# Kernel tuning notes

Hardware: AMD Instinct MI355X
Metric: run time of the kernel (lower is better)

Reference implementation:

```python
import jax, jax.numpy as jnp
import numpy as np

H, W = 32, 56
CK, CV = 64, 512
N = 16 * H * W  # long + work memory fully populated: 16 frames of H*W entries
TOP_K = 30


def setup_inputs() -> dict:
    key = jax.random.key(0)
    k1, k2, k3, k4, k5 = jax.random.split(key, 5)
    return {
        "q_key": jax.random.normal(k1, (1, CK, H, W), dtype=jnp.float32),
        "q_selection": jax.random.uniform(k2, (1, CK, H, W), dtype=jnp.float32),
        "mem_key": jax.random.normal(k3, (1, CK, N), dtype=jnp.float32),
        "mem_shrinkage": jax.random.uniform(k4, (1, N, 1), dtype=jnp.float32),
        "mem_value": jax.random.normal(k5, (2, CV, N), dtype=jnp.float32),
    }


def reference(q_key, q_selection, mem_key, mem_shrinkage, mem_value):
    b, ck, h, w = q_key.shape
    hw = h * w
    qk = q_key.reshape(1, ck, hw)          # [1, CK, HW]
    qs = q_selection.reshape(1, ck, hw)    # [1, CK, HW]

    mk = jnp.swapaxes(mem_key, 1, 2)       # [1, N, CK]
    # negative weighted squared L2 distance via matmul algebra
    a_sq = jnp.matmul(mk * mk, qs)                    # [1, N, HW]
    two_ab = 2.0 * jnp.matmul(mk, qk * qs)            # [1, N, HW]
    b_sq = jnp.sum(qs * qk * qk, axis=1, keepdims=True)  # [1, 1, HW]
    sim = (-a_sq + two_ab - b_sq) * mem_shrinkage / jnp.sqrt(jnp.float32(ck))  # [1, N, HW]

    # topk over the memory axis (dim=1), softmax over selected entries, scatter back
    simT = jnp.swapaxes(sim, 1, 2)                    # [1, HW, N]
    vals, idx = jax.lax.top_k(simT, TOP_K)            # [1, HW, K]
    x_exp = jnp.exp(vals)
    x_exp = x_exp / jnp.sum(x_exp, axis=-1, keepdims=True)
    i0 = jnp.arange(1)[:, None, None]
    i1 = jnp.arange(hw)[None, :, None]
    affT = jnp.zeros_like(simT).at[i0, i1, idx].set(x_exp)  # [1, HW, N]
    affinity = jnp.swapaxes(affT, 1, 2)               # [1, N, HW]

    out = jnp.matmul(mem_value, affinity)             # [2, CV, HW] (batch-broadcast)
    return out.reshape(2, CV, h, w)
```

## Files before the change

### kernel.cpp

```cpp
#include <hip/hip_runtime.h>
#include <math.h>

#define HW      1792
#define NMEM    28672
#define NCHUNK  3584
#define TOPK    30
#define KSEL    48
#define SCAP    64
#define SIMB    448
#define WPS     7

typedef __attribute__((ext_vector_type(8))) short bf16x8;
typedef __attribute__((ext_vector_type(8))) unsigned short u16x8;
typedef __attribute__((ext_vector_type(4))) float f32x4;
typedef __attribute__((ext_vector_type(4))) _Float16 h4;
typedef unsigned long long ull;

static __device__ __forceinline__ unsigned short f2bf(float v) {
  unsigned b = __float_as_uint(v);
  return (unsigned short)((b + 0x7FFFu + ((b >> 16) & 1u)) >> 16);
}
static __device__ __forceinline__ float bf2f(unsigned short h) {
  return __uint_as_float(((unsigned)h) << 16);
}
static __device__ __forceinline__ unsigned fkey(float v) {
  return __float_as_uint(-v) & 0x7FFFFFFFu;
}
static __device__ __forceinline__ ull umax64(ull a, ull b) { return a > b ? a : b; }
static __device__ __forceinline__ ull umin64(ull a, ull b) { return a < b ? a : b; }
static __device__ __forceinline__ void gl_lds16(const void* g, void* l) {
  __builtin_amdgcn_global_load_lds(
      (const __attribute__((address_space(1))) unsigned*)g,
      (__attribute__((address_space(3))) unsigned*)l, 16, 0, 0);
}
#define WSYNC() do { asm volatile("s_waitcnt lgkmcnt(0)" ::: "memory"); \
                     __builtin_amdgcn_wave_barrier(); } while (0)

__global__ __launch_bounds__(256)
void k_prep_b(const float* __restrict__ mk, const float* __restrict__ shr_in,
              unsigned short* __restrict__ Bh,
              float* __restrict__ mkT, float* __restrict__ shr_s)
{
  const int n = blockIdx.x * 256 + threadIdx.x;
  shr_s[n] = shr_in[n] * 0.125f;
  for (int cb = 0; cb < 64; cb += 8) {
    u16x8 h1, h2;
    float vv[8];
    #pragma unroll
    for (int j = 0; j < 8; ++j) {
      float v = mk[(size_t)(cb + j) * NMEM + n];
      vv[j] = v;
      h1[j] = f2bf(v);
      h2[j] = f2bf(v * v);
    }
    const int s = cb >> 3;
    *reinterpret_cast<u16x8*>(&Bh[((size_t)s * NMEM + n) * 8])       = h1;
    *reinterpret_cast<u16x8*>(&Bh[((size_t)(s + 8) * NMEM + n) * 8]) = h2;
    *reinterpret_cast<float4*>(&mkT[(size_t)n * 64 + cb])     = make_float4(vv[0], vv[1], vv[2], vv[3]);
    *reinterpret_cast<float4*>(&mkT[(size_t)n * 64 + cb + 4]) = make_float4(vv[4], vv[5], vv[6], vv[7]);
  }
}

__global__ __launch_bounds__(256)
void k_prep_u(const float* __restrict__ q_key, const float* __restrict__ q_sel,
              unsigned short* __restrict__ Uh, unsigned short* __restrict__ Ul,
              float* __restrict__ bsq)
{
  const int p = blockIdx.x * 256 + threadIdx.x;
  float bs = 0.f;
  for (int cb = 0; cb < 64; cb += 8) {
    u16x8 h1, l1, h2, l2;
    #pragma unroll
    for (int j = 0; j < 8; ++j) {
      int c = cb + j;
      float k = q_key[(size_t)c * HW + p];
      float s = q_sel[(size_t)c * HW + p];
      float u = 2.f * k * s;
      float w = -s;
      bs = fmaf(s * k, k, bs);
      unsigned short h = f2bf(u); h1[j] = h; l1[j] = f2bf(u - bf2f(h));
      unsigned short g = f2bf(w); h2[j] = g; l2[j] = f2bf(w - bf2f(g));
    }
    const int s = cb >> 3;
    *reinterpret_cast<u16x8*>(&Uh[((size_t)s * HW + p) * 8])       = h1;
    *reinterpret_cast<u16x8*>(&Ul[((size_t)s * HW + p) * 8])       = l1;
    *reinterpret_cast<u16x8*>(&Uh[((size_t)(s + 8) * HW + p) * 8]) = h2;
    *reinterpret_cast<u16x8*>(&Ul[((size_t)(s + 8) * HW + p) * 8]) = l2;
  }
  bsq[p] = bs;
}

__global__ __launch_bounds__(256, 2)
void k_sim(const unsigned short* __restrict__ Uh, const unsigned short* __restrict__ Ul,
           const unsigned short* __restrict__ Bh,
           const float* __restrict__ bsq, const float* __restrict__ shr_s,
           float* __restrict__ pmax)
{
  __shared__ char smem[65536] __attribute__((aligned(16)));
  const int tid = threadIdx.x;
  const int wid = tid >> 6, lane = tid & 63;
  const int lr = lane & 15, lg = lane >> 4;
  const int pb = blockIdx.x % 14, st = blockIdx.x / 14;
  const int pw = pb * 128 + wid * 32;
  const int w0 = st * WPS;

  bf16x8 a0h[4], a0l[4], a1h[4], a1l[4];
  #pragma unroll
  for (int t = 0; t < 4; ++t) {
    const size_t e0 = ((size_t)(t * 4 + lg) * HW + pw + lr) * 8;
    const size_t e1 = e0 + 16 * 8;
    a0h[t] = *reinterpret_cast<const bf16x8*>(&Uh[e0]);
    a0l[t] = *reinterpret_cast<const bf16x8*>(&Ul[e0]);
    a1h[t] = *reinterpret_cast<const bf16x8*>(&Uh[e1]);
    a1l[t] = *reinterpret_cast<const bf16x8*>(&Ul[e1]);
  }
  float bq[2][4];
  #pragma unroll
  for (int pt = 0; pt < 2; ++pt)
    #pragma unroll
    for (int r = 0; r < 4; ++r) bq[pt][r] = bsq[pw + pt * 16 + 4 * lg + r];

  auto stage = [&](int buf, int i) {
    const int n0 = (w0 + i) * 128;
    #pragma unroll
    for (int j = 0; j < 8; ++j) {
      const int idx = j * 256 + tid;
      const int s = idx >> 7, rr = idx & 127;
      gl_lds16((const char*)Bh + ((size_t)s * NMEM + n0 + rr) * 16,
               smem + buf * 32768 + idx * 16);
    }
  };

  stage(0, 0);
  int buf = 0;
  for (int i = 0; i < WPS; ++i) {
    __syncthreads();
    if (i + 1 < WPS) stage(buf ^ 1, i + 1);

    f32x4 acc[2][8];
    #pragma unroll
    for (int a = 0; a < 2; ++a)
      #pragma unroll
      for (int b = 0; b < 8; ++b) acc[a][b] = (f32x4){0.f, 0.f, 0.f, 0.f};

    const short* lb = (const short*)(smem + buf * 32768);
    #pragma unroll
    for (int t = 0; t < 4; ++t) {
      #pragma unroll
      for (int nt = 0; nt < 8; ++nt) {
        bf16x8 bh = *reinterpret_cast<const bf16x8*>(
            &lb[((t * 4 + lg) * 128 + nt * 16 + lr) * 8]);
        acc[0][nt] = __builtin_amdgcn_mfma_f32_16x16x32_bf16(a0h[t], bh, acc[0][nt], 0, 0, 0);
        acc[0][nt] = __builtin_amdgcn_mfma_f32_16x16x32_bf16(a0l[t], bh, acc[0][nt], 0, 0, 0);
        acc[1][nt] = __builtin_amdgcn_mfma_f32_16x16x32_bf16(a1h[t], bh, acc[1][nt], 0, 0, 0);
        acc[1][nt] = __builtin_amdgcn_mfma_f32_16x16x32_bf16(a1l[t], bh, acc[1][nt], 0, 0, 0);
      }
    }

    const int wgl = w0 + i;
    const int n0 = wgl * 128;
    float shv[8];
    #pragma unroll
    for (int nt = 0; nt < 8; ++nt) shv[nt] = shr_s[n0 + nt * 16 + lr];
    #pragma unroll
    for (int pt = 0; pt < 2; ++pt) {
      #pragma unroll
      for (int r = 0; r < 4; ++r) {
        float mx = -INFINITY;
        #pragma unroll
        for (int nt = 0; nt < 8; ++nt)
          mx = fmaxf(mx, (acc[pt][nt][r] - bq[pt][r]) * shv[nt]);
        pmax[(size_t)(pw + pt * 16 + 4 * lg + r) * NCHUNK + wgl * 16 + lr] = mx;
      }
    }
    buf ^= 1;
  }
}

__global__ __launch_bounds__(256, 2)
void k_select(const float* __restrict__ pmax, const float* __restrict__ mkT,
              const float* __restrict__ q_key, const float* __restrict__ q_sel,
              const float* __restrict__ shr_s,
              float* __restrict__ wgt, int* __restrict__ widx)
{
  __shared__ ull   cand[4][512];
  __shared__ ull   fin[4][256];
  __shared__ short sl[4][SCAP];
  __shared__ float sqk[4][64], sqs[4][64];

  const int w = threadIdx.x >> 6, lane = threadIdx.x & 63;
  const int pix = blockIdx.x * 4 + w;
  ull*   cd = cand[w];
  ull*   fn = fin[w];
  short* sv = sl[w];

  sqk[w][lane] = q_key[(size_t)lane * HW + pix];
  sqs[w][lane] = q_sel[(size_t)lane * HW + pix];

  const float* pm = pmax + (size_t)pix * NCHUNK;

  float t0 = -INFINITY, t1 = -INFINITY, t2 = -INFINITY, t3 = -INFINITY;
  #pragma unroll
  for (int j = 0; j < 56; ++j) {
    float v = pm[lane + 64 * j];
    if (v > t3) {
      if (v > t1) {
        t3 = t2; t2 = t1;
        if (v > t0) { t1 = t0; t0 = v; } else t1 = v;
      } else {
        t3 = t2;
        if (v > t2) t2 = v; else t3 = v;
      }
    }
  }
  const unsigned u0 = fkey(t0), u1 = fkey(t1), u2 = fkey(t2), u3 = fkey(t3);

  unsigned lo = 0, hi = 0x7FFFFFFFu;
  while (lo < hi) {
    unsigned mid = (lo + hi) >> 1;
    int c = (u0 <= mid) + (u1 <= mid) + (u2 <= mid) + (u3 <= mid);
    int tot = __popcll(__ballot(c >= 1)) + __popcll(__ballot(c >= 2)) +
              __popcll(__ballot(c >= 3)) + __popcll(__ballot(c >= 4));
    if (tot >= KSEL) hi = mid; else lo = mid + 1;
  }
  const unsigned T48 = lo;

  int ns = 0;
  #pragma unroll
  for (int j = 0; j < 56; ++j) {
    bool keep = (fkey(pm[lane + 64 * j]) <= T48);
    ull ball = __ballot(keep);
    if (keep) {
      int pos = ns + __popcll(ball & ((1ull << lane) - 1ull));
      if (pos < SCAP) sv[pos] = (short)(lane + 64 * j);
    }
    ns += __popcll(ball);
  }
  ns = (ns < SCAP) ? ns : SCAP;
  const int NC = ns * 8;
  WSYNC();

  const float4* k4p = reinterpret_cast<const float4*>(sqk[w]);
  const float4* s4p = reinterpret_cast<const float4*>(sqs[w]);
  ull myp[8];
  #pragma unroll
  for (int i = 0; i < 8; ++i) {
    myp[i] = 0ull;
    const int c = lane + (i << 6);
    if (c < NC) {
      const int cc = sv[c >> 3];
      const int n = ((cc >> 4) << 7) + (cc & 15) + ((c & 7) << 4);
      const float4* mr = reinterpret_cast<const float4*>(mkT + (size_t)n * 64);
      float s0 = 0.f, s1 = 0.f, s2 = 0.f, s3 = 0.f;
      #pragma unroll
      for (int j = 0; j < 4; ++j) {
        float4 q0 = mr[4*j], q1 = mr[4*j+1], q2 = mr[4*j+2], q3 = mr[4*j+3];
        float4 a0 = k4p[4*j], a1 = k4p[4*j+1], a2 = k4p[4*j+2], a3 = k4p[4*j+3];
        float4 b0 = s4p[4*j], b1 = s4p[4*j+1], b2 = s4p[4*j+2], b3 = s4p[4*j+3];
        float d;
        d = q0.x-a0.x; s0 = fmaf(b0.x*d, d, s0);
        d = q0.y-a0.y; s1 = fmaf(b0.y*d, d, s1);
        d = q0.z-a0.z; s2 = fmaf(b0.z*d, d, s2);
        d = q0.w-a0.w; s3 = fmaf(b0.w*d, d, s3);
        d = q1.x-a1.x; s0 = fmaf(b1.x*d, d, s0);
        d = q1.y-a1.y; s1 = fmaf(b1.y*d, d, s1);
        d = q1.z-a1.z; s2 = fmaf(b1.z*d, d, s2);
        d = q1.w-a1.w; s3 = fmaf(b1.w*d, d, s3);
        d = q2.x-a2.x; s0 = fmaf(b2.x*d, d, s0);
        d = q2.y-a2.y; s1 = fmaf(b2.y*d, d, s1);
        d = q2.z-a2.z; s2 = fmaf(b2.z*d, d, s2);
        d = q2.w-a2.w; s3 = fmaf(b2.w*d, d, s3);
        d = q3.x-a3.x; s0 = fmaf(b3.x*d, d, s0);
        d = q3.y-a3.y; s1 = fmaf(b3.y*d, d, s1);
        d = q3.z-a3.z; s2 = fmaf(b3.z*d, d, s2);
        d = q3.w-a3.w; s3 = fmaf(b3.w*d, d, s3);
      }
      float svv = -((s0 + s1) + (s2 + s3)) * shr_s[n];
      myp[i] = ((ull)(0x7FFFFFFFu - fkey(svv)) << 32) |
               (ull)(0xFFFFFFFFu - (unsigned)n);
    }
    cd[lane + (i << 6)] = myp[i];
  }
  WSYNC();

  ull p0 = 0, p1 = 0, p2 = 0, p3 = 0;
  #pragma unroll
  for (int i = 0; i < 8; ++i) {
    ull k = myp[i], m;
    m = umax64(p0, k); k = umin64(p0, k); p0 = m;
    m = umax64(p1, k); k = umin64(p1, k); p1 = m;
    m = umax64(p2, k); k = umin64(p2, k); p2 = m;
    m = umax64(p3, k); k = umin64(p3, k); p3 = m;
  }
  fn[lane * 4 + 0] = p0; fn[lane * 4 + 1] = p1;
  fn[lane * 4 + 2] = p2; fn[lane * 4 + 3] = p3;
  WSYNC();

  int r0 = 0, r1 = 0, r2 = 0, r3 = 0;
  for (int k = 0; k < 256; ++k) {
    ull kb = fn[k];
    r0 += (kb > p0); r1 += (kb > p1); r2 += (kb > p2); r3 += (kb > p3);
  }
  ull c30 = (r0 == TOPK - 1) ? p0 : (r1 == TOPK - 1) ? p1 :
            (r2 == TOPK - 1) ? p2 : (r3 == TOPK - 1) ? p3 : 0ull;
  ull ball2 = __ballot(c30 != 0ull);
  ull k30 = __shfl(c30, (int)(__ffsll((long long)ball2) - 1));

  int cnt = 0;
  #pragma unroll
  for (int i = 0; i < 8; ++i) cnt += (myp[i] > k30);
  #pragma unroll
  for (int off = 32; off > 0; off >>= 1) cnt += __shfl_xor(cnt, off);
  const bool ok = (cnt == TOPK - 1);

  if (ok) {
    float v0 = -__uint_as_float(0x7FFFFFFFu - (unsigned)(p0 >> 32));
    float v1 = -__uint_as_float(0x7FFFFFFFu - (unsigned)(p1 >> 32));
    float v2 = -__uint_as_float(0x7FFFFFFFu - (unsigned)(p2 >> 32));
    float v3 = -__uint_as_float(0x7FFFFFFFu - (unsigned)(p3 >> 32));
    float e0 = (r0 < TOPK) ? expf(v0) : 0.f;
    float e1 = (r1 < TOPK) ? expf(v1) : 0.f;
    float e2 = (r2 < TOPK) ? expf(v2) : 0.f;
    float e3 = (r3 < TOPK) ? expf(v3) : 0.f;
    float es = e0 + e1 + e2 + e3;
    #pragma unroll
    for (int off = 32; off > 0; off >>= 1) es += __shfl_xor(es, off);
    if (r0 < TOPK) { wgt[(size_t)pix*32 + r0] = e0/es; widx[(size_t)pix*32 + r0] = (int)(0xFFFFFFFFu - (unsigned)(p0 & 0xFFFFFFFFu)); }
    if (r1 < TOPK) { wgt[(size_t)pix*32 + r1] = e1/es; widx[(size_t)pix*32 + r1] = (int)(0xFFFFFFFFu - (unsigned)(p1 & 0xFFFFFFFFu)); }
    if (r2 < TOPK) { wgt[(size_t)pix*32 + r2] = e2/es; widx[(size_t)pix*32 + r2] = (int)(0xFFFFFFFFu - (unsigned)(p2 & 0xFFFFFFFFu)); }
    if (r3 < TOPK) { wgt[(size_t)pix*32 + r3] = e3/es; widx[(size_t)pix*32 + r3] = (int)(0xFFFFFFFFu - (unsigned)(p3 & 0xFFFFFFFFu)); }
  } else {
    int rr[8];
    #pragma unroll
    for (int i = 0; i < 8; ++i) rr[i] = 0;
    for (int k = 0; k < NC; ++k) {
      ull kb = cd[k];
      #pragma unroll
      for (int i = 0; i < 8; ++i) rr[i] += (kb > myp[i]);
    }
    float ev[8]; float es = 0.f;
    #pragma unroll
    for (int i = 0; i < 8; ++i) {
      float vv = -__uint_as_float(0x7FFFFFFFu - (unsigned)(myp[i] >> 32));
      ev[i] = (myp[i] != 0ull && rr[i] < TOPK) ? expf(vv) : 0.f;
      es += ev[i];
    }
    #pragma unroll
    for (int off = 32; off > 0; off >>= 1) es += __shfl_xor(es, off);
    #pragma unroll
    for (int i = 0; i < 8; ++i) {
      if (myp[i] != 0ull && rr[i] < TOPK) {
        wgt [(size_t)pix * 32 + rr[i]] = ev[i] / es;
        widx[(size_t)pix * 32 + rr[i]] = (int)(0xFFFFFFFFu - (unsigned)(myp[i] & 0xFFFFFFFFu));
      }
    }
  }
}

__global__ __launch_bounds__(256)
void k_transpose_h(const float* __restrict__ mv, _Float16* __restrict__ mvT)
{
  __shared__ float t[64][65];
  const int n0 = blockIdx.x * 64, ch0 = blockIdx.y * 64;
  const int tid = threadIdx.x;
  for (int i = tid; i < 64 * 16; i += 256) {
    int r = i >> 4, c4 = (i & 15) << 2;
    float4 v = *reinterpret_cast<const float4*>(&mv[(size_t)(ch0 + r) * NMEM + n0 + c4]);
    t[r][c4] = v.x; t[r][c4 + 1] = v.y; t[r][c4 + 2] = v.z; t[r][c4 + 3] = v.w;
  }
  __syncthreads();
  for (int i = tid; i < 64 * 16; i += 256) {
    int r = i >> 4, c4 = (i & 15) << 2;
    h4 hv = {(_Float16)t[c4][r], (_Float16)t[c4 + 1][r],
             (_Float16)t[c4 + 2][r], (_Float16)t[c4 + 3][r]};
    *reinterpret_cast<h4*>(&mvT[(size_t)(n0 + r) * 1024 + ch0 + c4]) = hv;
  }
}

__global__ __launch_bounds__(256)
void k_gather_h(const _Float16* __restrict__ mvT, const float* __restrict__ wgt,
                const int* __restrict__ widx, float* __restrict__ out)
{
  __shared__ float sw[8][TOPK];
  __shared__ int   si[8][TOPK];
  __shared__ float sbuf[256][9];
  const int p0 = blockIdx.x * 8, chg = blockIdx.y * 256;
  const int tid = threadIdx.x;

  for (int i = tid; i < 8 * TOPK; i += 256) {
    int q = i / TOPK, k = i - q * TOPK;
    sw[q][k] = wgt [(size_t)(p0 + q) * 32 + k];
    si[q][k] = widx[(size_t)(p0 + q) * 32 + k];
  }
  __syncthreads();

  const int ch = chg + tid;
  #pragma unroll 2
  for (int q = 0; q < 8; ++q) {
    float a = 0.f;
    #pragma unroll
    for (int k = 0; k < TOPK; ++k)
      a = fmaf(sw[q][k], (float)mvT[(size_t)si[q][k] * 1024 + ch], a);
    sbuf[tid][q] = a;
  }
  __syncthreads();

  for (int i = tid; i < 256 * 8; i += 256) {
    int cl = i >> 3, q = i & 7;
    out[(size_t)(chg + cl) * HW + p0 + q] = sbuf[cl][q];
  }
}

__global__ __launch_bounds__(256)
void k_gather_f(const float* __restrict__ src, const float* __restrict__ wgt,
                const int* __restrict__ widx, float* __restrict__ out,
                long n_stride, long ch_stride)
{
  __shared__ float sw[8][TOPK];
  __shared__ int   si[8][TOPK];
  __shared__ float sbuf[256][9];
  const int p0 = blockIdx.x * 8, chg = blockIdx.y * 256;
  const int tid = threadIdx.x;

  for (int i = tid; i < 8 * TOPK; i += 256) {
    int q = i / TOPK, k = i - q * TOPK;
    sw[q][k] = wgt [(size_t)(p0 + q) * 32 + k];
    si[q][k] = widx[(size_t)(p0 + q) * 32 + k];
  }
  __syncthreads();

  const int ch = chg + tid;
  #pragma unroll 2
  for (int q = 0; q < 8; ++q) {
    float a = 0.f;
    #pragma unroll
    for (int k = 0; k < TOPK; ++k)
      a = fmaf(sw[q][k], src[(size_t)si[q][k] * n_stride + (size_t)ch * ch_stride], a);
    sbuf[tid][q] = a;
  }
  __syncthreads();

  for (int i = tid; i < 256 * 8; i += 256) {
    int cl = i >> 3, q = i & 7;
    out[(size_t)(chg + cl) * HW + p0 + q] = sbuf[cl][q];
  }
}

extern "C" void kernel_launch(void* const* d_in, const int* in_sizes, int n_in,
                              void* d_out, int out_size, void* d_ws, size_t ws_size,
                              hipStream_t stream)
{
  (void)in_sizes; (void)n_in; (void)out_size;
  const float* q_key     = (const float*)d_in[0];
  const float* q_sel     = (const float*)d_in[1];
  const float* mem_key   = (const float*)d_in[2];
  const float* mem_shr   = (const float*)d_in[3];
  const float* mem_value = (const float*)d_in[4];
  float* out = (float*)d_out;

  char* ws = (char*)d_ws;
  size_t off = 0;
  auto alloc = [&](size_t b) { size_t c = off; off = (off + b + 255) & ~(size_t)255; return c; };
  size_t o_w   = alloc((size_t)HW * 32 * 4);
  size_t o_wi  = alloc((size_t)HW * 32 * 4);
  size_t o_pr  = off;
  size_t o_bh  = alloc((size_t)NMEM * 128 * 2);
  size_t o_uh  = alloc((size_t)HW * 128 * 2);
  size_t o_ul  = alloc((size_t)HW * 128 * 2);
  size_t o_bsq = alloc((size_t)HW * 4);
  size_t o_shr = alloc((size_t)NMEM * 4);
  size_t o_mkT = alloc((size_t)NMEM * 64 * 4);
  size_t o_pm  = alloc((size_t)HW * NCHUNK * 4);
  size_t o_end = off;

  float*          wg   = (float*)(ws + o_w);
  int*            wi   = (int*)  (ws + o_wi);
  unsigned short* Bh   = (unsigned short*)(ws + o_bh);
  unsigned short* Uh   = (unsigned short*)(ws + o_uh);
  unsigned short* Ul   = (unsigned short*)(ws + o_ul);
  float*          bsq  = (float*)(ws + o_bsq);
  float*          shr  = (float*)(ws + o_shr);
  float*          mkT  = (float*)(ws + o_mkT);
  float*          pmx  = (float*)(ws + o_pm);

  const size_t mvh_sz = (size_t)NMEM * 1024 * 2;

  k_prep_b<<<NMEM / 256, 256, 0, stream>>>(mem_key, mem_shr, Bh, mkT, shr);
  k_prep_u<<<HW / 256, 256, 0, stream>>>(q_key, q_sel, Uh, Ul, bsq);
  k_sim<<<SIMB, 256, 0, stream>>>(Uh, Ul, Bh, bsq, shr, pmx);

  if (ws_size >= o_end + mvh_sz) {
    _Float16* mvT = (_Float16*)(ws + o_end);
    k_transpose_h<<<dim3(NMEM / 64, 16), 256, 0, stream>>>(mem_value, mvT);
    k_select<<<HW / 4, 256, 0, stream>>>(pmx, mkT, q_key, q_sel, shr, wg, wi);
    k_gather_h<<<dim3(HW / 8, 4), 256, 0, stream>>>(mvT, wg, wi, out);
  } else if (ws_size >= o_pr + mvh_sz) {
    k_select<<<HW / 4, 256, 0, stream>>>(pmx, mkT, q_key, q_sel, shr, wg, wi);
    _Float16* mvT = (_Float16*)(ws + o_pr);
    k_transpose_h<<<dim3(NMEM / 64, 16), 256, 0, stream>>>(mem_value, mvT);
    k_gather_h<<<dim3(HW / 8, 4), 256, 0, stream>>>(mvT, wg, wi, out);
  } else {
    k_select<<<HW / 4, 256, 0, stream>>>(pmx, mkT, q_key, q_sel, shr, wg, wi);
    k_gather_f<<<dim3(HW / 8, 4), 256, 0, stream>>>(
        mem_value, wg, wi, out, 1, NMEM);
  }
}
```

Baseline: 153.2 us.

## Merge prep kernels and co-schedule value transpose inside similarity kernel

```diff
diff --git a/kernel.cpp b/kernel.cpp
--- a/kernel.cpp
+++ b/kernel.cpp
@@ -37,70 +37,97 @@
                      __builtin_amdgcn_wave_barrier(); } while (0)
 
 __global__ __launch_bounds__(256)
-void k_prep_b(const float* __restrict__ mk, const float* __restrict__ shr_in,
-              unsigned short* __restrict__ Bh,
-              float* __restrict__ mkT, float* __restrict__ shr_s)
-{
-  const int n = blockIdx.x * 256 + threadIdx.x;
-  shr_s[n] = shr_in[n] * 0.125f;
-  for (int cb = 0; cb < 64; cb += 8) {
-    u16x8 h1, h2;
-    float vv[8];
-    #pragma unroll
-    for (int j = 0; j < 8; ++j) {
-      float v = mk[(size_t)(cb + j) * NMEM + n];
-      vv[j] = v;
-      h1[j] = f2bf(v);
-      h2[j] = f2bf(v * v);
-    }
-    const int s = cb >> 3;
-    *reinterpret_cast<u16x8*>(&Bh[((size_t)s * NMEM + n) * 8])       = h1;
-    *reinterpret_cast<u16x8*>(&Bh[((size_t)(s + 8) * NMEM + n) * 8]) = h2;
-    *reinterpret_cast<float4*>(&mkT[(size_t)n * 64 + cb])     = make_float4(vv[0], vv[1], vv[2], vv[3]);
-    *reinterpret_cast<float4*>(&mkT[(size_t)n * 64 + cb + 4]) = make_float4(vv[4], vv[5], vv[6], vv[7]);
-  }
-}
-
-__global__ __launch_bounds__(256)
-void k_prep_u(const float* __restrict__ q_key, const float* __restrict__ q_sel,
-              unsigned short* __restrict__ Uh, unsigned short* __restrict__ Ul,
-              float* __restrict__ bsq)
-{
-  const int p = blockIdx.x * 256 + threadIdx.x;
-  float bs = 0.f;
-  for (int cb = 0; cb < 64; cb += 8) {
-    u16x8 h1, l1, h2, l2;
-    #pragma unroll
-    for (int j = 0; j < 8; ++j) {
-      int c = cb + j;
-      float k = q_key[(size_t)c * HW + p];
-      float s = q_sel[(size_t)c * HW + p];
-      float u = 2.f * k * s;
-      float w = -s;
-      bs = fmaf(s * k, k, bs);
-      unsigned short h = f2bf(u); h1[j] = h; l1[j] = f2bf(u - bf2f(h));
-      unsigned short g = f2bf(w); h2[j] = g; l2[j] = f2bf(w - bf2f(g));
-    }
-    const int s = cb >> 3;
-    *reinterpret_cast<u16x8*>(&Uh[((size_t)s * HW + p) * 8])       = h1;
-    *reinterpret_cast<u16x8*>(&Ul[((size_t)s * HW + p) * 8])       = l1;
-    *reinterpret_cast<u16x8*>(&Uh[((size_t)(s + 8) * HW + p) * 8]) = h2;
-    *reinterpret_cast<u16x8*>(&Ul[((size_t)(s + 8) * HW + p) * 8]) = l2;
-  }
-  bsq[p] = bs;
+void k_prep(const float* __restrict__ mk, const float* __restrict__ shr_in,
+            const float* __restrict__ q_key, const float* __restrict__ q_sel,
+            unsigned short* __restrict__ Bh,
+            unsigned short* __restrict__ Uh, unsigned short* __restrict__ Ul,
+            float* __restrict__ mkT, float* __restrict__ shr_s,
+            float* __restrict__ bsq)
+{
+  if (blockIdx.x < NMEM / 256) {
+    const int n = blockIdx.x * 256 + threadIdx.x;
+    shr_s[n] = shr_in[n] * 0.125f;
+    for (int cb = 0; cb < 64; cb += 8) {
+      u16x8 h1, h2;
+      float vv[8];
+      #pragma unroll
+      for (int j = 0; j < 8; ++j) {
+        float v = mk[(size_t)(cb + j) * NMEM + n];
+        vv[j] = v;
+        h1[j] = f2bf(v);
+        h2[j] = f2bf(v * v);
+      }
+      const int s = cb >> 3;
+      *reinterpret_cast<u16x8*>(&Bh[((size_t)s * NMEM + n) * 8])       = h1;
+      *reinterpret_cast<u16x8*>(&Bh[((size_t)(s + 8) * NMEM + n) * 8]) = h2;
+      *reinterpret_cast<float4*>(&mkT[(size_t)n * 64 + cb])     = make_float4(vv[0], vv[1], vv[2], vv[3]);
+      *reinterpret_cast<float4*>(&mkT[(size_t)n * 64 + cb + 4]) = make_float4(vv[4], vv[5], vv[6], vv[7]);
+    }
+  } else {
+    const int p = (blockIdx.x - NMEM / 256) * 256 + threadIdx.x;
+    float bs = 0.f;
+    for (int cb = 0; cb < 64; cb += 8) {
+      u16x8 h1, l1, h2, l2;
+      #pragma unroll
+      for (int j = 0; j < 8; ++j) {
+        int c = cb + j;
+        float k = q_key[(size_t)c * HW + p];
+        float s = q_sel[(size_t)c * HW + p];
+        float u = 2.f * k * s;
+        float w = -s;
+        bs = fmaf(s * k, k, bs);
+        unsigned short h = f2bf(u); h1[j] = h; l1[j] = f2bf(u - bf2f(h));
+        unsigned short g = f2bf(w); h2[j] = g; l2[j] = f2bf(w - bf2f(g));
+      }
+      const int s = cb >> 3;
+      *reinterpret_cast<u16x8*>(&Uh[((size_t)s * HW + p) * 8])       = h1;
+      *reinterpret_cast<u16x8*>(&Ul[((size_t)s * HW + p) * 8])       = l1;
+      *reinterpret_cast<u16x8*>(&Uh[((size_t)(s + 8) * HW + p) * 8]) = h2;
+      *reinterpret_cast<u16x8*>(&Ul[((size_t)(s + 8) * HW + p) * 8]) = l2;
+    }
+    bsq[p] = bs;
+  }
 }
 
 __global__ __launch_bounds__(256, 2)
-void k_sim(const unsigned short* __restrict__ Uh, const unsigned short* __restrict__ Ul,
-           const unsigned short* __restrict__ Bh,
-           const float* __restrict__ bsq, const float* __restrict__ shr_s,
-           float* __restrict__ pmax)
+void k_simT(const unsigned short* __restrict__ Uh, const unsigned short* __restrict__ Ul,
+            const unsigned short* __restrict__ Bh,
+            const float* __restrict__ bsq, const float* __restrict__ shr_s,
+            float* __restrict__ pmax,
+            const float* __restrict__ mv, _Float16* __restrict__ mvT)
 {
   __shared__ char smem[65536] __attribute__((aligned(16)));
   const int tid = threadIdx.x;
+
+  int sb = -1, tb = -1;
+  if (gridDim.x > SIMB) {
+    const int g = blockIdx.x / 17, r = blockIdx.x % 17;
+    if (r == 0) sb = g; else tb = g * 16 + (r - 1);
+  } else {
+    sb = blockIdx.x;
+  }
+
+  if (tb >= 0) {
+    float (*tt)[65] = (float(*)[65])smem;
+    const int n0 = (tb % 448) * 64, ch0 = (tb / 448) * 64;
+    for (int i = tid; i < 64 * 16; i += 256) {
+      int r = i >> 4, c4 = (i & 15) << 2;
+      float4 v = *reinterpret_cast<const float4*>(&mv[(size_t)(ch0 + r) * NMEM + n0 + c4]);
+      tt[r][c4] = v.x; tt[r][c4 + 1] = v.y; tt[r][c4 + 2] = v.z; tt[r][c4 + 3] = v.w;
+    }
+    __syncthreads();
+    for (int i = tid; i < 64 * 16; i += 256) {
+      int r = i >> 4, c4 = (i & 15) << 2;
+      h4 hv = {(_Float16)tt[c4][r], (_Float16)tt[c4 + 1][r],
+               (_Float16)tt[c4 + 2][r], (_Float16)tt[c4 + 3][r]};
+      *reinterpret_cast<h4*>(&mvT[(size_t)(n0 + r) * 1024 + ch0 + c4]) = hv;
+    }
+    return;
+  }
+
   const int wid = tid >> 6, lane = tid & 63;
   const int lr = lane & 15, lg = lane >> 4;
-  const int pb = blockIdx.x % 14, st = blockIdx.x / 14;
+  const int pb = sb % 14, st = sb / 14;
   const int pw = pb * 128 + wid * 32;
   const int w0 = st * WPS;
 
@@ -485,21 +512,25 @@
 
   const size_t mvh_sz = (size_t)NMEM * 1024 * 2;
 
-  k_prep_b<<<NMEM / 256, 256, 0, stream>>>(mem_key, mem_shr, Bh, mkT, shr);
-  k_prep_u<<<HW / 256, 256, 0, stream>>>(q_key, q_sel, Uh, Ul, bsq);
-  k_sim<<<SIMB, 256, 0, stream>>>(Uh, Ul, Bh, bsq, shr, pmx);
+  k_prep<<<NMEM / 256 + HW / 256, 256, 0, stream>>>(
+      mem_key, mem_shr, q_key, q_sel, Bh, Uh, Ul, mkT, shr, bsq);
 
   if (ws_size >= o_end + mvh_sz) {
     _Float16* mvT = (_Float16*)(ws + o_end);
-    k_transpose_h<<<dim3(NMEM / 64, 16), 256, 0, stream>>>(mem_value, mvT);
+    k_simT<<<SIMB * 17, 256, 0, stream>>>(Uh, Ul, Bh, bsq, shr, pmx,
+                                          mem_value, mvT);
     k_select<<<HW / 4, 256, 0, stream>>>(pmx, mkT, q_key, q_sel, shr, wg, wi);
     k_gather_h<<<dim3(HW / 8, 4), 256, 0, stream>>>(mvT, wg, wi, out);
   } else if (ws_size >= o_pr + mvh_sz) {
+    k_simT<<<SIMB, 256, 0, stream>>>(Uh, Ul, Bh, bsq, shr, pmx,
+                                     mem_value, nullptr);
     k_select<<<HW / 4, 256, 0, stream>>>(pmx, mkT, q_key, q_sel, shr, wg, wi);
     _Float16* mvT = (_Float16*)(ws + o_pr);
     k_transpose_h<<<dim3(NMEM / 64, 16), 256, 0, stream>>>(mem_value, mvT);
     k_gather_h<<<dim3(HW / 8, 4), 256, 0, stream>>>(mvT, wg, wi, out);
   } else {
+    k_simT<<<SIMB, 256, 0, stream>>>(Uh, Ul, Bh, bsq, shr, pmx,
+                                     mem_value, nullptr);
     k_select<<<HW / 4, 256, 0, stream>>>(pmx, mkT, q_key, q_sel, shr, wg, wi);
     k_gather_f<<<dim3(HW / 8, 4), 256, 0, stream>>>(
         mem_value, wg, wi, out, 1, NMEM);
```

Measured after the change: 157.1 us. +2.5%, slower.
